# Optimization experiments

Hardware: AMD Instinct MI355X
Metric: run time of the kernel (lower is better)

## Reference

```python
import jax, jax.numpy as jnp
import numpy as np

HIDDEN = 384
NDIM = 3
N_POINTS = 100000
N_SUPER = 2048
MAX_DEG = 32
RADIUS = 0.045
INPUT_DIM = 3


def _sincos_embed(coords):
    # ContinuousSincosEmbed: dim=384, ndim=3 -> 128 channels per spatial dim (64 sin + 64 cos)
    eff = HIDDEN // NDIM  # 128
    omega = jnp.arange(0, eff, 2, dtype=jnp.float32) / eff
    freq = 1.0 / (10000.0 ** omega)  # [eff//2]
    out = coords[..., None] * freq  # [..., ndim, eff//2]
    emb = jnp.concatenate([jnp.sin(out), jnp.cos(out)], axis=-1)  # [..., ndim, eff]
    return emb.reshape(coords.shape[:-1] + (HIDDEN,))


def _radius_neighbors(pos, sn_idx):
    # numpy preprocessing equivalent of torch_geometric.nn.pool.radius with
    # max_num_neighbors=MAX_DEG; fixed-size padded [S, K] output + validity mask.
    nbr = np.zeros((N_SUPER, MAX_DEG), np.int32)
    mask = np.zeros((N_SUPER, MAX_DEG), bool)
    pos2 = (pos ** 2).sum(-1)
    r2 = RADIUS * RADIUS
    chunk = 128
    for i0 in range(0, N_SUPER, chunk):
        sp = pos[sn_idx[i0:i0 + chunk]]
        d2 = (sp ** 2).sum(-1)[:, None] + pos2[None, :] - 2.0 * (sp @ pos.T)
        within = d2 <= r2
        for j in range(sp.shape[0]):
            idx = np.nonzero(within[j])[0][:MAX_DEG]
            nbr[i0 + j, :len(idx)] = idx
            mask[i0 + j, :len(idx)] = True
    return nbr, mask


def setup_inputs() -> dict:
    rng = np.random.default_rng(0)
    pos = rng.random((N_POINTS, NDIM)).astype(np.float32)
    sn_idx = np.sort(rng.choice(N_POINTS, N_SUPER, replace=False)).astype(np.int32)
    nbr, mask = _radius_neighbors(pos, sn_idx)
    key = jax.random.key(0)
    ks = jax.random.split(key, 6)
    s = 0.02  # truncnormal002 init scale
    return {
        "input_pos": jnp.asarray(pos),
        "input_feat": jax.random.normal(ks[0], (N_POINTS, INPUT_DIM), jnp.float32),
        "supernode_idx": jnp.asarray(sn_idx),
        "neighbor_idx": jnp.asarray(nbr),
        "neighbor_mask": jnp.asarray(mask),
        "W_in": jax.random.normal(ks[1], (INPUT_DIM, HIDDEN), jnp.float32) * s,
        "b_in": jnp.zeros((HIDDEN,), jnp.float32),
        "W1": jax.random.normal(ks[2], (2 * HIDDEN, HIDDEN), jnp.float32) * s,
        "b1": jnp.zeros((HIDDEN,), jnp.float32),
        "W2": jax.random.normal(ks[3], (HIDDEN, HIDDEN), jnp.float32) * s,
        "b2": jnp.zeros((HIDDEN,), jnp.float32),
        "W_proj": jax.random.normal(ks[4], (2 * HIDDEN, HIDDEN), jnp.float32) * s,
        "b_proj": jnp.zeros((HIDDEN,), jnp.float32),
    }


def reference(input_pos, input_feat, supernode_idx, neighbor_idx, neighbor_mask,
              W_in, b_in, W1, b1, W2, b2, W_proj, b_proj):
    # point embeddings: continuous sincos pos embed + input feature projection
    x = _sincos_embed(input_pos) + input_feat @ W_in + b_in          # [N, D]
    sn = x[supernode_idx]                                            # [S, D] supernode pos embed
    src = x[neighbor_idx]                                            # [S, K, D] gathered neighbors
    dst = jnp.broadcast_to(sn[:, None, :], src.shape)                # [S, K, D]
    h = jnp.concatenate([src, dst], axis=-1)                         # [S, K, 2D]
    # message MLP (Linear -> GELU(exact) -> Linear), as nn.GELU default
    h = jax.nn.gelu(h @ W1 + b1, approximate=False) @ W2 + b2        # [S, K, D]
    # masked mean == segment_csr(..., reduce='mean') over variable-degree edges
    m = neighbor_mask[..., None].astype(h.dtype)
    agg = (h * m).sum(axis=1) / jnp.maximum(m.sum(axis=1), 1.0)      # [S, D]
    # readd_supernode_pos: concat supernode pos embed, project 2D -> D
    out = jnp.concatenate([agg, sn], axis=-1) @ W_proj + b_proj      # [S, D]
    return out[None]                                                 # [1, S, D] (batch_size=1)
```

## Files before the change

kernel.cpp:

```cpp
#include <hip/hip_runtime.h>
#include <hip/hip_bf16.h>
#include <cstdint>

#define HIDDEN 384
#define NSUPER 2048
#define FRAGS (12*24*64)
#define WBLK  (FRAGS*8)

typedef __attribute__((ext_vector_type(8))) short bf16x8;
typedef __attribute__((ext_vector_type(4))) float f32x4;

__device__ inline unsigned short f2bf(float f) {
    unsigned int u = __float_as_uint(f);
    return (unsigned short)((u + 0x7fffu + ((u >> 16) & 1u)) >> 16);
}
__device__ inline bf16x8 pack8(const float* v) {
    union { bf16x8 v8; unsigned short u[8]; } u;
    #pragma unroll
    for (int i = 0; i < 8; ++i) u.u[i] = f2bf(v[i]);
    return u.v8;
}
__device__ inline float gelu(float y) {
    const float y2 = y * y;
    const float m  = __expf(y * fmaf(-0.0713548163f, y2, -1.5957691216f));
    return y * (1.0f / (1.0f + m));
}

__global__ __launch_bounds__(256)
void prep(const float* __restrict__ W1, const float* __restrict__ W2,
          const float* __restrict__ Wp, const unsigned int* __restrict__ mask,
          const float* __restrict__ pos, const float* __restrict__ feat,
          const int* __restrict__ sn_idx,
          const float* __restrict__ W_in, const float* __restrict__ b_in,
          unsigned short* __restrict__ w1sf, unsigned short* __restrict__ w1df,
          unsigned short* __restrict__ w2f,  unsigned short* __restrict__ wpf,
          unsigned short* __restrict__ snxb, int* __restrict__ flag) {
    const int b = blockIdx.x;
    const int t = threadIdx.x;
    if (b == 360) {
        __shared__ int s;
        if (t == 0) s = 0;
        __syncthreads();
        int bad = 0;
        for (int i = t; i < 16384; i += 256)
            if (mask[i] > 1u) bad = 1;
        if (bad) s = 1;
        __syncthreads();
        if (t == 0) *flag = s;
        return;
    }
    if (b > 360) {
        __shared__ float W4[HIDDEN][4];
        __shared__ float P6[64][7];
        const int eb = b - 361;
        if (t < 64) {
            const int pi = sn_idx[eb*64 + t];
            P6[t][0]=pos[pi*3];  P6[t][1]=pos[pi*3+1];  P6[t][2]=pos[pi*3+2];
            P6[t][3]=feat[pi*3]; P6[t][4]=feat[pi*3+1]; P6[t][5]=feat[pi*3+2];
        }
        for (int d = t; d < HIDDEN; d += 256) {
            W4[d][0]=W_in[d]; W4[d][1]=W_in[HIDDEN+d];
            W4[d][2]=W_in[2*HIDDEN+d]; W4[d][3]=b_in[d];
        }
        __syncthreads();
        const int er = t >> 2, seg = t & 3;
        float frA[8], frB[8];
        #pragma unroll
        for (int i = 0; i < 8; ++i) {
            frA[i] = exp2f(-(float)(seg*8 + i)      * 0.2076205059304601f);
            frB[i] = exp2f(-(float)(32 + seg*8 + i) * 0.2076205059304601f);
        }
        const float f0 = P6[er][3], f1 = P6[er][4], f2 = P6[er][5];
        #pragma unroll
        for (int cc = 0; cc < 3; ++cc) {
            const float pc = P6[er][cc];
            float sL[8], sH[8], cL[8], cH[8];
            #pragma unroll
            for (int i = 0; i < 8; ++i) {
                const float aL = pc*frA[i], aH = pc*frB[i];
                sL[i]=__sinf(aL); sH[i]=__sinf(aH); cL[i]=__cosf(aL); cH[i]=__cosf(aH);
            }
            #pragma unroll
            for (int q = 0; q < 4; ++q) {
                const float* bb = (q==0)?sL:(q==1)?sH:(q==2)?cL:cH;
                const int blk = cc*4 + q;
                float v[8];
                #pragma unroll
                for (int i = 0; i < 8; ++i) {
                    const int dim = blk*32 + seg*8 + i;
                    const float4 wv = *(const float4*)W4[dim];
                    v[i] = fmaf(f0, wv.x, fmaf(f1, wv.y, fmaf(f2, wv.z, bb[i] + wv.w)));
                }
                *(bf16x8*)&snxb[(size_t)(eb*64 + er)*HIDDEN + blk*32 + seg*8] = pack8(v);
            }
        }
        return;
    }
    const int grp = b / 72, sub = b % 72;
    const float* W; unsigned short* out;
    switch (grp) {
        case 0: W = W1;              out = w1sf; break;
        case 1: W = W1 + 384*HIDDEN; out = w1df; break;
        case 2: W = W2;              out = w2f;  break;
        case 3: W = Wp;              out = wpf;  break;
        default:W = Wp + 384*HIDDEN; out = wpf + WBLK; break;
    }
    const int idx = sub * 256 + t;
    const int l   = idx & 63;
    const int frag= idx >> 6;
    const int nt  = frag % 24;
    const int kt  = frag / 24;
    const int col = nt * 16 + (l & 15);
    const int k0  = kt * 32 + (l >> 4) * 8;
    unsigned int pk[4];
    #pragma unroll
    for (int j = 0; j < 4; ++j) {
        unsigned int lo = f2bf(W[(size_t)(k0 + 2*j)     * HIDDEN + col]);
        unsigned int hi = f2bf(W[(size_t)(k0 + 2*j + 1) * HIDDEN + col]);
        pk[j] = lo | (hi << 16);
    }
    *reinterpret_cast<uint4*>(&out[(size_t)idx * 8]) =
        *reinterpret_cast<const uint4*>(pk);
}

__global__ __launch_bounds__(256)
void k_dstv(const unsigned short* __restrict__ snxb,
            const unsigned short* __restrict__ w1df,
            const float* __restrict__ b1, float* __restrict__ dstv) {
    const int rg = blockIdx.x >> 2, cq = blockIdx.x & 3;
    const int t = threadIdx.x, w = t>>6, l = t&63, lg = l>>4, l15 = l&15;
    const int wgm = w>>1, wgn = w&1;
    const int r0 = rg*64 + wgm*32;
    const int ntb = cq*6 + wgn*3;
    f32x4 acc[2][3];
    #pragma unroll
    for (int mt=0; mt<2; ++mt)
        #pragma unroll
        for (int nt=0; nt<3; ++nt) acc[mt][nt] = (f32x4){0.f,0.f,0.f,0.f};
    #pragma unroll 2
    for (int kt = 0; kt < 12; ++kt) {
        bf16x8 a[2], bfr[3];
        const unsigned short* bpp = &w1df[((size_t)(kt*24 + ntb)*64 + l)*8];
        #pragma unroll
        for (int nt=0; nt<3; ++nt) bfr[nt] = *(const bf16x8*)(bpp + (size_t)nt*512);
        #pragma unroll
        for (int mt=0; mt<2; ++mt)
            a[mt] = *(const bf16x8*)&snxb[(size_t)(r0 + mt*16 + l15)*HIDDEN + kt*32 + lg*8];
        #pragma unroll
        for (int mt=0; mt<2; ++mt)
            #pragma unroll
            for (int nt=0; nt<3; ++nt)
                acc[mt][nt] = __builtin_amdgcn_mfma_f32_16x16x32_bf16(a[mt], bfr[nt], acc[mt][nt], 0,0,0);
    }
    #pragma unroll
    for (int mt=0; mt<2; ++mt)
        #pragma unroll
        for (int nt=0; nt<3; ++nt) {
            const int col = cq*96 + wgn*48 + nt*16 + l15;
            #pragma unroll
            for (int r=0; r<4; ++r) {
                const int row = r0 + mt*16 + lg*4 + r;
                dstv[(size_t)row*HIDDEN + col] = acc[mt][nt][r] + b1[col];
            }
        }
}

__global__ __launch_bounds__(512, 2)
void k_mlp(const float* __restrict__ pos, const float* __restrict__ feat,
           const int* __restrict__ nbr_idx, const void* __restrict__ mask_raw,
           const int* __restrict__ mask_fmt,
           const float* __restrict__ W_in, const float* __restrict__ b_in,
           const float* __restrict__ dstv,
           const unsigned short* __restrict__ W1sf,
           unsigned short* __restrict__ aggpre, float* __restrict__ cntf)
{
    __shared__ unsigned short G[8*12*64*8];
    __shared__ float4 WINT[HIDDEN];
    __shared__ float PF[128][7];
    __shared__ float CNT[4];

    const int t  = threadIdx.x;
    const int bm = blockIdx.x;
    const int l = t & 63, w = t >> 6;
    const int mg = w >> 2, ng = w & 3;
    const int lg = l >> 4, l15 = l & 15;

    float dvreg[2][6];
    #pragma unroll
    for (int sl = 0; sl < 2; ++sl)
        #pragma unroll
        for (int nt = 0; nt < 6; ++nt)
            dvreg[sl][nt] = dstv[(size_t)(bm*4 + mg*2 + sl)*HIDDEN + ng*96 + nt*16 + l15];

    if (t < 128) {
        const int e  = bm*128 + t;
        const int pi = nbr_idx[e];
        PF[t][0]=pos[pi*3];  PF[t][1]=pos[pi*3+1];  PF[t][2]=pos[pi*3+2];
        PF[t][3]=feat[pi*3]; PF[t][4]=feat[pi*3+1]; PF[t][5]=feat[pi*3+2];
        const int fmt = *mask_fmt;
        const int mv  = fmt ? (int)((const unsigned char*)mask_raw)[e]
                            : ((const int*)mask_raw)[e];
        PF[t][6] = mv ? 1.0f : 0.0f;
    }
    if (t >= 128 && t < 128 + HIDDEN) {
        const int d = t - 128;
        WINT[d] = (float4){W_in[d], W_in[HIDDEN+d], W_in[2*HIDDEN+d], b_in[d]};
    }
    __syncthreads();
    if (t < 4) {
        float c = 0.f;
        for (int s = 0; s < 32; ++s) c += PF[t*32+s][6];
        CNT[t] = c;
    }

    {
        const int er = t >> 2, seg = t & 3;
        float frA[8], frB[8];
        #pragma unroll
        for (int i = 0; i < 8; ++i) {
            frA[i] = exp2f(-(float)(seg*8 + i)      * 0.2076205059304601f);
            frB[i] = exp2f(-(float)(32 + seg*8 + i) * 0.2076205059304601f);
        }
        const float f0 = PF[er][3], f1 = PF[er][4], f2 = PF[er][5];
        const float pc0 = PF[er][0], pc1 = PF[er][1], pc2 = PF[er][2];
        const int slotbase = (er>>4)*12*64 + seg*16 + (er&15);
        #pragma unroll
        for (int kt = 0; kt < 12; ++kt) {
            const float pc = (kt>>2)==0 ? pc0 : ((kt>>2)==1 ? pc1 : pc2);
            float v[8];
            #pragma unroll
            for (int i = 0; i < 8; ++i) {
                const float fr = (kt&1) ? frB[i] : frA[i];
                const float aa = pc * fr;
                const float base = ((kt>>1)&1) ? __cosf(aa) : __sinf(aa);
                const float4 wv = WINT[kt*32 + seg*8 + i];
                v[i] = fmaf(f0, wv.x, fmaf(f1, wv.y, fmaf(f2, wv.z, base + wv.w)));
            }
            *(bf16x8*)&G[(size_t)(slotbase + kt*64)*8] = pack8(v);
        }
    }
    __syncthreads();

    f32x4 acc[4][6];
    #pragma unroll
    for (int mt=0; mt<4; ++mt)
        #pragma unroll
        for (int nt=0; nt<6; ++nt) acc[mt][nt] = (f32x4){0.f,0.f,0.f,0.f};

    bf16x8 bA[6], bB[6];
    #define LOADB(dst, kt)                                                      \
        { const unsigned short* bp_ = &W1sf[((size_t)((kt)*24 + ng*6)*64 + l)*8];\
          _Pragma("unroll")                                                     \
          for (int nt_ = 0; nt_ < 6; ++nt_)                                     \
              dst[nt_] = *(const bf16x8*)(bp_ + (size_t)nt_*512); }
    #define AREAD(a_, kt)                                                       \
        { _Pragma("unroll")                                                     \
          for (int mt_ = 0; mt_ < 4; ++mt_)                                     \
              a_[mt_] = *(const bf16x8*)&G[(size_t)((((mg*4 + mt_)*12 + (kt))*64) + l)*8]; }
    #define MFMA6(bfr, a_)                                                      \
        { __builtin_amdgcn_s_setprio(1);                                        \
          _Pragma("unroll")                                                     \
          for (int mt_ = 0; mt_ < 4; ++mt_)                                     \
              _Pragma("unroll")                                                 \
              for (int nt_ = 0; nt_ < 6; ++nt_)                                 \
                  acc[mt_][nt_] = __builtin_amdgcn_mfma_f32_16x16x32_bf16(      \
                      a_[mt_], bfr[nt_], acc[mt_][nt_], 0, 0, 0);               \
          __builtin_amdgcn_s_setprio(0); }

    LOADB(bA, 0); LOADB(bB, 1);
    #pragma unroll
    for (int kt = 0; kt < 12; kt += 2) {
        bf16x8 a[4];
        AREAD(a, kt);
        MFMA6(bA, a);
        if (kt + 2 < 12) LOADB(bA, kt + 2);
        AREAD(a, kt + 1);
        MFMA6(bB, a);
        if (kt + 3 < 12) LOADB(bB, kt + 3);
    }

    float mvr[4][4];
    #pragma unroll
    for (int mt=0; mt<4; ++mt)
        #pragma unroll
        for (int r=0; r<4; ++r)
            mvr[mt][r] = PF[(mg*4 + mt)*16 + lg*4 + r][6];
    #pragma unroll
    for (int nt=0; nt<6; ++nt) {
        const int col = ng*96 + nt*16 + l15;
        float s0 = 0.f, s1 = 0.f;
        #pragma unroll
        for (int mt=0; mt<4; ++mt) {
            const float dv = dvreg[mt>>1][nt];
            float p = 0.f;
            #pragma unroll
            for (int r=0; r<4; ++r)
                p += mvr[mt][r] * gelu(acc[mt][nt][r] + dv);
            if (mt < 2) s0 += p; else s1 += p;
        }
        s0 += __shfl_xor(s0,16); s0 += __shfl_xor(s0,32);
        s1 += __shfl_xor(s1,16); s1 += __shfl_xor(s1,32);
        if (lg == 0) {
            const int sn0 = bm*4 + mg*2;
            aggpre[(size_t)sn0*HIDDEN + col]     = f2bf(s0 / fmaxf(CNT[mg*2],1.f));
            aggpre[(size_t)(sn0+1)*HIDDEN + col] = f2bf(s1 / fmaxf(CNT[mg*2+1],1.f));
        }
    }
    if (t < 4) cntf[bm*4 + t] = CNT[t];
    #undef LOADB
    #undef AREAD
    #undef MFMA6
}

__global__ __launch_bounds__(256)
void k_out(const unsigned short* __restrict__ aggpre,
           const unsigned short* __restrict__ snxb,
           const unsigned short* __restrict__ w2f,
           const unsigned short* __restrict__ wpf,
           const float* __restrict__ b2, const float* __restrict__ bp,
           const float* __restrict__ cntf, float* __restrict__ out) {
    __shared__ unsigned short AGG[64][392];
    const int rg = blockIdx.x >> 2, cq = blockIdx.x & 3;
    const int t = threadIdx.x, w = t>>6, l = t&63, lg = l>>4, l15 = l&15;
    const int wgm = w>>1, wgn = w&1;
    const int r0g = rg*64;

    {
        const int rowm = wgm*32;
        f32x4 acc[2][12];
        #pragma unroll
        for (int mt=0; mt<2; ++mt)
            #pragma unroll
            for (int nt=0; nt<12; ++nt) acc[mt][nt] = (f32x4){0.f,0.f,0.f,0.f};
        for (int kt = 0; kt < 12; ++kt) {
            bf16x8 a[2], bfr[12];
            const unsigned short* bpp = &w2f[((size_t)(kt*24 + wgn*12)*64 + l)*8];
            #pragma unroll
            for (int nt=0; nt<12; ++nt) bfr[nt] = *(const bf16x8*)(bpp + (size_t)nt*512);
            #pragma unroll
            for (int mt=0; mt<2; ++mt)
                a[mt] = *(const bf16x8*)&aggpre[(size_t)(r0g + rowm + mt*16 + l15)*HIDDEN + kt*32 + lg*8];
            #pragma unroll
            for (int mt=0; mt<2; ++mt)
                #pragma unroll
                for (int nt=0; nt<12; ++nt)
                    acc[mt][nt] = __builtin_amdgcn_mfma_f32_16x16x32_bf16(a[mt], bfr[nt], acc[mt][nt], 0,0,0);
        }
        #pragma unroll
        for (int mt=0; mt<2; ++mt)
            #pragma unroll
            for (int nt=0; nt<12; ++nt) {
                const int col = wgn*192 + nt*16 + l15;
                const float bb = b2[col];
                #pragma unroll
                for (int r=0; r<4; ++r) {
                    const int row = rowm + mt*16 + lg*4 + r;
                    const float nz = (cntf[r0g + row] > 0.f) ? 1.f : 0.f;
                    AGG[row][col] = f2bf(acc[mt][nt][r] + bb*nz);
                }
            }
    }
    __syncthreads();

    const int r0 = r0g + wgm*32;
    const int ntb = cq*6 + wgn*3;
    f32x4 acc[2][3];
    #pragma unroll
    for (int mt=0; mt<2; ++mt)
        #pragma unroll
        for (int nt=0; nt<3; ++nt) acc[mt][nt] = (f32x4){0.f,0.f,0.f,0.f};
    #pragma unroll 2
    for (int kt = 0; kt < 24; ++kt) {
        const unsigned short* Wb = (kt < 12) ? wpf : wpf + WBLK;
        const int ktt = (kt < 12) ? kt : kt - 12;
        bf16x8 a[2], bfr[3];
        const unsigned short* bpp = &Wb[((size_t)(ktt*24 + ntb)*64 + l)*8];
        #pragma unroll
        for (int nt=0; nt<3; ++nt) bfr[nt] = *(const bf16x8*)(bpp + (size_t)nt*512);
        #pragma unroll
        for (int mt=0; mt<2; ++mt) {
            if (kt < 12)
                a[mt] = *(const bf16x8*)&AGG[wgm*32 + mt*16 + l15][ktt*32 + lg*8];
            else
                a[mt] = *(const bf16x8*)&snxb[(size_t)(r0 + mt*16 + l15)*HIDDEN + ktt*32 + lg*8];
        }
        #pragma unroll
        for (int mt=0; mt<2; ++mt)
            #pragma unroll
            for (int nt=0; nt<3; ++nt)
                acc[mt][nt] = __builtin_amdgcn_mfma_f32_16x16x32_bf16(a[mt], bfr[nt], acc[mt][nt], 0,0,0);
    }
    #pragma unroll
    for (int mt=0; mt<2; ++mt)
        #pragma unroll
        for (int nt=0; nt<3; ++nt) {
            const int col = cq*96 + wgn*48 + nt*16 + l15;
            #pragma unroll
            for (int r=0; r<4; ++r) {
                const int row = r0 + mt*16 + lg*4 + r;
                out[(size_t)row*HIDDEN + col] = acc[mt][nt][r] + bp[col];
            }
        }
}

extern "C" void kernel_launch(void* const* d_in, const int* in_sizes, int n_in,
                              void* d_out, int out_size, void* d_ws, size_t ws_size,
                              hipStream_t stream) {
    const float* pos   = (const float*)d_in[0];
    const float* feat  = (const float*)d_in[1];
    const int*   sn    = (const int*)d_in[2];
    const int*   nbr   = (const int*)d_in[3];
    const void*  mask  = d_in[4];
    const float* W_in  = (const float*)d_in[5];
    const float* b_in  = (const float*)d_in[6];
    const float* W1    = (const float*)d_in[7];
    const float* b1    = (const float*)d_in[8];
    const float* W2    = (const float*)d_in[9];
    const float* b2    = (const float*)d_in[10];
    const float* Wp    = (const float*)d_in[11];
    const float* bpv   = (const float*)d_in[12];
    float* out = (float*)d_out;

    char* base = (char*)d_ws;
    int* flag = (int*)base;
    unsigned short* w1sf = (unsigned short*)(base + 256);
    unsigned short* w1df = w1sf + WBLK;
    unsigned short* w2f  = w1df + WBLK;
    unsigned short* wpf  = w2f  + WBLK;
    unsigned short* snxb = wpf  + 2*(size_t)WBLK;
    unsigned short* aggp = snxb + (size_t)NSUPER*HIDDEN;
    float* cntf = (float*)(aggp + (size_t)NSUPER*HIDDEN);
    float* dstv = cntf + NSUPER;

    hipLaunchKernelGGL(prep, dim3(393), dim3(256), 0, stream,
                       W1, W2, Wp, (const unsigned int*)mask,
                       pos, feat, sn, W_in, b_in,
                       w1sf, w1df, w2f, wpf, snxb, flag);
    hipLaunchKernelGGL(k_dstv, dim3(128), dim3(256), 0, stream,
                       snxb, w1df, b1, dstv);
    hipLaunchKernelGGL(k_mlp, dim3(512), dim3(512), 0, stream,
                       pos, feat, nbr, mask, flag, W_in, b_in, dstv,
                       w1sf, aggp, cntf);
    hipLaunchKernelGGL(k_out, dim3(128), dim3(256), 0, stream,
                       aggp, snxb, w2f, wpf, b2, bpv, cntf, out);
}
```

Before: 89.62 us.

## Switch message-MLP GEMM to 32x32x16 MFMA with 1024-thread blocks

The main edge GEMM in k_mlp moves from 16x16x32 MFMA tiles to 32x32x16 tiles. W1's source half is repacked in prep into a matching 32-column fragment layout, and the embedding staging in LDS is rewritten to fill 32-row A fragments. Blocks grow to 1024 threads, with each wave owning one supernode (32 edges) and 96 output columns. The intent is fewer MFMA instructions and less per-wave A/B fragment traffic. In exchange each wave holds 48 accumulator registers, and the larger block may cut occupancy.

```diff
diff --git a/kernel.cpp b/kernel.cpp
--- a/kernel.cpp
+++ b/kernel.cpp
@@ -4,11 +4,11 @@
 
 #define HIDDEN 384
 #define NSUPER 2048
-#define FRAGS (12*24*64)
-#define WBLK  (FRAGS*8)
-
-typedef __attribute__((ext_vector_type(8))) short bf16x8;
-typedef __attribute__((ext_vector_type(4))) float f32x4;
+#define WBLK  (12*24*64*8)
+
+typedef __attribute__((ext_vector_type(8)))  short bf16x8;
+typedef __attribute__((ext_vector_type(4)))  float f32x4;
+typedef __attribute__((ext_vector_type(16))) float f32x16;
 
 __device__ inline unsigned short f2bf(float f) {
     unsigned int u = __float_as_uint(f);
@@ -32,7 +32,7 @@
           const float* __restrict__ pos, const float* __restrict__ feat,
           const int* __restrict__ sn_idx,
           const float* __restrict__ W_in, const float* __restrict__ b_in,
-          unsigned short* __restrict__ w1sf, unsigned short* __restrict__ w1df,
+          unsigned short* __restrict__ w1s32, unsigned short* __restrict__ w1df,
           unsigned short* __restrict__ w2f,  unsigned short* __restrict__ wpf,
           unsigned short* __restrict__ snxb, int* __restrict__ flag) {
     const int b = blockIdx.x;
@@ -97,21 +97,27 @@
         return;
     }
     const int grp = b / 72, sub = b % 72;
-    const float* W; unsigned short* out;
-    switch (grp) {
-        case 0: W = W1;              out = w1sf; break;
-        case 1: W = W1 + 384*HIDDEN; out = w1df; break;
-        case 2: W = W2;              out = w2f;  break;
-        case 3: W = Wp;              out = wpf;  break;
-        default:W = Wp + 384*HIDDEN; out = wpf + WBLK; break;
-    }
     const int idx = sub * 256 + t;
     const int l   = idx & 63;
     const int frag= idx >> 6;
-    const int nt  = frag % 24;
-    const int kt  = frag / 24;
-    const int col = nt * 16 + (l & 15);
-    const int k0  = kt * 32 + (l >> 4) * 8;
+    const float* W; unsigned short* out;
+    int col, k0;
+    if (grp == 0) {
+        W = W1; out = w1s32;
+        const int nt = frag % 12, kt = frag / 12;
+        col = nt*32 + (l & 31);
+        k0  = kt*16 + (l >> 5)*8;
+    } else {
+        switch (grp) {
+            case 1: W = W1 + 384*HIDDEN; out = w1df; break;
+            case 2: W = W2;              out = w2f;  break;
+            case 3: W = Wp;              out = wpf;  break;
+            default:W = Wp + 384*HIDDEN; out = wpf + WBLK; break;
+        }
+        const int nt = frag % 24, kt = frag / 24;
+        col = nt*16 + (l & 15);
+        k0  = kt*32 + (l >> 4)*8;
+    }
     unsigned int pk[4];
     #pragma unroll
     for (int j = 0; j < 4; ++j) {
@@ -165,17 +171,17 @@
         }
 }
 
-__global__ __launch_bounds__(512, 2)
+__global__ __launch_bounds__(1024)
 void k_mlp(const float* __restrict__ pos, const float* __restrict__ feat,
            const int* __restrict__ nbr_idx, const void* __restrict__ mask_raw,
            const int* __restrict__ mask_fmt,
            const float* __restrict__ W_in, const float* __restrict__ b_in,
            const float* __restrict__ dstv,
-           const unsigned short* __restrict__ W1sf,
+           const unsigned short* __restrict__ W1s32,
            unsigned short* __restrict__ aggpre, float* __restrict__ cntf)
 {
-    __shared__ unsigned short G[8*12*64*8];
-    __shared__ float4 WINT[HIDDEN];
+    __shared__ unsigned short G[4*24*64*8];
+    __shared__ float WIN0[HIDDEN], WIN1[HIDDEN], WIN2[HIDDEN], WINB[HIDDEN];
     __shared__ float PF[128][7];
     __shared__ float CNT[4];
 
@@ -183,14 +189,6 @@
     const int bm = blockIdx.x;
     const int l = t & 63, w = t >> 6;
     const int mg = w >> 2, ng = w & 3;
-    const int lg = l >> 4, l15 = l & 15;
-
-    float dvreg[2][6];
-    #pragma unroll
-    for (int sl = 0; sl < 2; ++sl)
-        #pragma unroll
-        for (int nt = 0; nt < 6; ++nt)
-            dvreg[sl][nt] = dstv[(size_t)(bm*4 + mg*2 + sl)*HIDDEN + ng*96 + nt*16 + l15];
 
     if (t < 128) {
         const int e  = bm*128 + t;
@@ -201,10 +199,10 @@
         const int mv  = fmt ? (int)((const unsigned char*)mask_raw)[e]
                             : ((const int*)mask_raw)[e];
         PF[t][6] = mv ? 1.0f : 0.0f;
-    }
-    if (t >= 128 && t < 128 + HIDDEN) {
+    } else if (t >= 128 && t < 128 + HIDDEN) {
         const int d = t - 128;
-        WINT[d] = (float4){W_in[d], W_in[HIDDEN+d], W_in[2*HIDDEN+d], b_in[d]};
+        WIN0[d] = W_in[d];          WIN1[d] = W_in[HIDDEN + d];
+        WIN2[d] = W_in[2*HIDDEN+d]; WINB[d] = b_in[d];
     }
     __syncthreads();
     if (t < 4) {
@@ -214,102 +212,95 @@
     }
 
     {
-        const int er = t >> 2, seg = t & 3;
-        float frA[8], frB[8];
-        #pragma unroll
-        for (int i = 0; i < 8; ++i) {
-            frA[i] = exp2f(-(float)(seg*8 + i)      * 0.2076205059304601f);
-            frB[i] = exp2f(-(float)(32 + seg*8 + i) * 0.2076205059304601f);
-        }
+        const int er = t >> 3, seg = t & 7;
+        float frS[8];
+        #pragma unroll
+        for (int j = 0; j < 8; ++j)
+            frS[j] = exp2f(-(float)(seg*8 + j) * 0.2076205059304601f);
         const float f0 = PF[er][3], f1 = PF[er][4], f2 = PF[er][5];
-        const float pc0 = PF[er][0], pc1 = PF[er][1], pc2 = PF[er][2];
-        const int slotbase = (er>>4)*12*64 + seg*16 + (er&15);
-        #pragma unroll
-        for (int kt = 0; kt < 12; ++kt) {
-            const float pc = (kt>>2)==0 ? pc0 : ((kt>>2)==1 ? pc1 : pc2);
-            float v[8];
-            #pragma unroll
-            for (int i = 0; i < 8; ++i) {
-                const float fr = (kt&1) ? frB[i] : frA[i];
-                const float aa = pc * fr;
-                const float base = ((kt>>1)&1) ? __cosf(aa) : __sinf(aa);
-                const float4 wv = WINT[kt*32 + seg*8 + i];
-                v[i] = fmaf(f0, wv.x, fmaf(f1, wv.y, fmaf(f2, wv.z, base + wv.w)));
-            }
-            *(bf16x8*)&G[(size_t)(slotbase + kt*64)*8] = pack8(v);
+        const float pcs[3] = {PF[er][0], PF[er][1], PF[er][2]};
+        const int lane = 32*(seg&1) + (er&31);
+        const int ktb  = seg >> 1;
+        const int mtb  = (er>>5)*24;
+        #pragma unroll
+        for (int cc = 0; cc < 3; ++cc) {
+            const float pc = pcs[cc];
+            #pragma unroll
+            for (int sc = 0; sc < 2; ++sc) {
+                const int kt = cc*8 + sc*4 + ktb;
+                float v[8];
+                #pragma unroll
+                for (int j = 0; j < 8; ++j) {
+                    const int dim = cc*128 + sc*64 + seg*8 + j;
+                    const float aa = pc * frS[j];
+                    const float base = sc ? __cosf(aa) : __sinf(aa);
+                    v[j] = fmaf(f0, WIN0[dim], fmaf(f1, WIN1[dim],
+                           fmaf(f2, WIN2[dim], base + WINB[dim])));
+                }
+                *(bf16x8*)&G[(size_t)((mtb + kt)*64 + lane)*8] = pack8(v);
+            }
         }
     }
     __syncthreads();
 
-    f32x4 acc[4][6];
-    #pragma unroll
-    for (int mt=0; mt<4; ++mt)
-        #pragma unroll
-        for (int nt=0; nt<6; ++nt) acc[mt][nt] = (f32x4){0.f,0.f,0.f,0.f};
-
-    bf16x8 bA[6], bB[6];
-    #define LOADB(dst, kt)                                                      \
-        { const unsigned short* bp_ = &W1sf[((size_t)((kt)*24 + ng*6)*64 + l)*8];\
-          _Pragma("unroll")                                                     \
-          for (int nt_ = 0; nt_ < 6; ++nt_)                                     \
+    f32x16 acc[3];
+    #pragma unroll
+    for (int nt = 0; nt < 3; ++nt)
+        #pragma unroll
+        for (int r = 0; r < 16; ++r) acc[nt][r] = 0.f;
+
+    bf16x8 bA[3], bB[3], aA, aB;
+    #define LOADB(dst, kt)                                                       \
+        { const unsigned short* bp_ = &W1s32[((size_t)((kt)*12 + ng*3)*64 + l)*8];\
+          _Pragma("unroll")                                                      \
+          for (int nt_ = 0; nt_ < 3; ++nt_)                                      \
               dst[nt_] = *(const bf16x8*)(bp_ + (size_t)nt_*512); }
-    #define AREAD(a_, kt)                                                       \
-        { _Pragma("unroll")                                                     \
-          for (int mt_ = 0; mt_ < 4; ++mt_)                                     \
-              a_[mt_] = *(const bf16x8*)&G[(size_t)((((mg*4 + mt_)*12 + (kt))*64) + l)*8]; }
-    #define MFMA6(bfr, a_)                                                      \
-        { __builtin_amdgcn_s_setprio(1);                                        \
-          _Pragma("unroll")                                                     \
-          for (int mt_ = 0; mt_ < 4; ++mt_)                                     \
-              _Pragma("unroll")                                                 \
-              for (int nt_ = 0; nt_ < 6; ++nt_)                                 \
-                  acc[mt_][nt_] = __builtin_amdgcn_mfma_f32_16x16x32_bf16(      \
-                      a_[mt_], bfr[nt_], acc[mt_][nt_], 0, 0, 0);               \
+    #define AREAD(kt) (*(const bf16x8*)&G[(size_t)((mg*24 + (kt))*64 + l)*8])
+    #define MFMA3(bfr, a_)                                                       \
+        { __builtin_amdgcn_s_setprio(1);                                         \
+          _Pragma("unroll")                                                      \
+          for (int nt_ = 0; nt_ < 3; ++nt_)                                      \
+              acc[nt_] = __builtin_amdgcn_mfma_f32_32x32x16_bf16(                \
+                  a_, bfr[nt_], acc[nt_], 0, 0, 0);                              \
           __builtin_amdgcn_s_setprio(0); }
 
     LOADB(bA, 0); LOADB(bB, 1);
-    #pragma unroll
-    for (int kt = 0; kt < 12; kt += 2) {
-        bf16x8 a[4];
-        AREAD(a, kt);
-        MFMA6(bA, a);
-        if (kt + 2 < 12) LOADB(bA, kt + 2);
-        AREAD(a, kt + 1);
-        MFMA6(bB, a);
-        if (kt + 3 < 12) LOADB(bB, kt + 3);
-    }
-
-    float mvr[4][4];
-    #pragma unroll
-    for (int mt=0; mt<4; ++mt)
-        #pragma unroll
-        for (int r=0; r<4; ++r)
-            mvr[mt][r] = PF[(mg*4 + mt)*16 + lg*4 + r][6];
-    #pragma unroll
-    for (int nt=0; nt<6; ++nt) {
-        const int col = ng*96 + nt*16 + l15;
-        float s0 = 0.f, s1 = 0.f;
-        #pragma unroll
-        for (int mt=0; mt<4; ++mt) {
-            const float dv = dvreg[mt>>1][nt];
-            float p = 0.f;
-            #pragma unroll
-            for (int r=0; r<4; ++r)
-                p += mvr[mt][r] * gelu(acc[mt][nt][r] + dv);
-            if (mt < 2) s0 += p; else s1 += p;
-        }
-        s0 += __shfl_xor(s0,16); s0 += __shfl_xor(s0,32);
-        s1 += __shfl_xor(s1,16); s1 += __shfl_xor(s1,32);
-        if (lg == 0) {
-            const int sn0 = bm*4 + mg*2;
-            aggpre[(size_t)sn0*HIDDEN + col]     = f2bf(s0 / fmaxf(CNT[mg*2],1.f));
-            aggpre[(size_t)(sn0+1)*HIDDEN + col] = f2bf(s1 / fmaxf(CNT[mg*2+1],1.f));
-        }
-    }
-    if (t < 4) cntf[bm*4 + t] = CNT[t];
+    aA = AREAD(0); aB = AREAD(1);
+    #pragma unroll
+    for (int kt = 0; kt < 24; kt += 2) {
+        MFMA3(bA, aA);
+        if (kt + 2 < 24) { LOADB(bA, kt + 2); aA = AREAD(kt + 2); }
+        MFMA3(bB, aB);
+        if (kt + 3 < 24) { LOADB(bB, kt + 3); aB = AREAD(kt + 3); }
+    }
     #undef LOADB
     #undef AREAD
-    #undef MFMA6
+    #undef MFMA3
+
+    const int lh = l >> 5, l31 = l & 31;
+    const int sn = bm*4 + mg;
+    float dv[3];
+    #pragma unroll
+    for (int nt = 0; nt < 3; ++nt)
+        dv[nt] = dstv[(size_t)sn*HIDDEN + ng*96 + nt*32 + l31];
+    float mvr[16];
+    #pragma unroll
+    for (int r = 0; r < 16; ++r) {
+        const int row = (r & 3) + 8*(r >> 2) + 4*lh;
+        mvr[r] = PF[mg*32 + row][6];
+    }
+    const float inv = 1.0f / fmaxf(CNT[mg], 1.f);
+    #pragma unroll
+    for (int nt = 0; nt < 3; ++nt) {
+        float s = 0.f;
+        #pragma unroll
+        for (int r = 0; r < 16; ++r)
+            s += mvr[r] * gelu(acc[nt][r] + dv[nt]);
+        s += __shfl_xor(s, 32);
+        if (lh == 0)
+            aggpre[(size_t)sn*HIDDEN + ng*96 + nt*32 + l31] = f2bf(s * inv);
+    }
+    if (t < 4) cntf[bm*4 + t] = CNT[t];
 }
 
 __global__ __launch_bounds__(256)
@@ -324,7 +315,6 @@
     const int t = threadIdx.x, w = t>>6, l = t&63, lg = l>>4, l15 = l&15;
     const int wgm = w>>1, wgn = w&1;
     const int r0g = rg*64;
-
     {
         const int rowm = wgm*32;
         f32x4 acc[2][12];
@@ -361,7 +351,6 @@
             }
     }
     __syncthreads();
-
     const int r0 = r0g + wgm*32;
     const int ntb = cq*6 + wgn*3;
     f32x4 acc[2][3];
@@ -423,8 +412,8 @@
 
     char* base = (char*)d_ws;
     int* flag = (int*)base;
-    unsigned short* w1sf = (unsigned short*)(base + 256);
-    unsigned short* w1df = w1sf + WBLK;
+    unsigned short* w1s32 = (unsigned short*)(base + 256);
+    unsigned short* w1df = w1s32 + WBLK;
     unsigned short* w2f  = w1df + WBLK;
     unsigned short* wpf  = w2f  + WBLK;
     unsigned short* snxb = wpf  + 2*(size_t)WBLK;
@@ -435,12 +424,12 @@
     hipLaunchKernelGGL(prep, dim3(393), dim3(256), 0, stream,
                        W1, W2, Wp, (const unsigned int*)mask,
                        pos, feat, sn, W_in, b_in,
-                       w1sf, w1df, w2f, wpf, snxb, flag);
+                       w1s32, w1df, w2f, wpf, snxb, flag);
     hipLaunchKernelGGL(k_dstv, dim3(128), dim3(256), 0, stream,
                        snxb, w1df, b1, dstv);
-    hipLaunchKernelGGL(k_mlp, dim3(512), dim3(512), 0, stream,
+    hipLaunchKernelGGL(k_mlp, dim3(512), dim3(1024), 0, stream,
                        pos, feat, nbr, mask, flag, W_in, b_in, dstv,
-                       w1sf, aggp, cntf);
+                       w1s32, aggp, cntf);
     hipLaunchKernelGGL(k_out, dim3(128), dim3(256), 0, stream,
                        aggp, snxb, w2f, wpf, b2, bpv, cntf, out);
 }
```

After: 92.49 us. +3.2%, slower.
